# Kernel tuning notes

Measured on AMD Instinct MI355X. Metric: run time of the kernel, lower is better.

Reference implementation:

```python
import jax, jax.numpy as jnp
import numpy as np

N_NODES = 100000
N_EDGES = 1600000
D = 128
BETA = 0.001
EPS = 1e-12  # F.normalize eps


def setup_inputs() -> dict:
    key = jax.random.key(0)
    k1, k2, k3, k4, k5, k6 = jax.random.split(key, 6)
    stdv = 1.0 / np.sqrt(D)
    return {
        "input": jax.random.normal(k1, (N_NODES, D), dtype=jnp.float32),
        "edge_rows": jax.random.randint(k2, (N_EDGES,), 0, N_NODES, dtype=jnp.int32),
        "edge_cols": jax.random.randint(k3, (N_EDGES,), 0, N_NODES, dtype=jnp.int32),
        "edge_vals": jax.random.uniform(k4, (N_EDGES,), dtype=jnp.float32),
        "weight": jax.random.uniform(k5, (D, D), minval=-stdv, maxval=stdv, dtype=jnp.float32),
        "bias": jax.random.uniform(k6, (D,), minval=-stdv, maxval=stdv, dtype=jnp.float32),
    }


def reference(input, edge_rows, edge_cols, edge_vals, weight, bias):
    # dense projection: [N, D]
    support = input @ weight
    # sparse neighbor aggregation: agg[i] = sum_{(i,j) in E} adj_val * support[j]
    msgs = edge_vals[:, None] * support[edge_cols]          # [E, D]
    agg = jax.ops.segment_sum(msgs, edge_rows, num_segments=input.shape[0])
    # beta-weighted residual blend
    out = BETA * input + (1.0 - BETA) * agg
    # row-wise L2 normalize (torch F.normalize, p=2, dim=1)
    norm = jnp.sqrt(jnp.sum(out * out, axis=1, keepdims=True))
    out = out / jnp.maximum(norm, EPS)
    # bias add
    return out + bias
```

## Files before the change

kernel.cpp:

```cpp
#include <hip/hip_runtime.h>

#define N_NODES 100000
#define N_EDGES 1600000
#define D 128
#define NB 1563
#define NSUB 8
#define SUBCAP 224
#define CAP (NSUB*SUBCAP)
#define EPT 8
#define SC_BLOCKS 782
#define CSTRIDE 16

typedef short bf16x8 __attribute__((ext_vector_type(8)));
typedef float f32x4 __attribute__((ext_vector_type(4)));

__device__ __forceinline__ unsigned short f2bf(float x){
  union { float f; unsigned u; } v; v.f = x;
  unsigned r = v.u + 0x7fffu + ((v.u >> 16) & 1u);
  return (unsigned short)(r >> 16);
}

__device__ __forceinline__ float bf2f(unsigned short h){
  union { unsigned u; float f; } v; v.u = ((unsigned)h) << 16;
  return v.f;
}

__global__ __launch_bounds__(256) void convert_input(const float4* __restrict__ in4,
                                                     ushort4* __restrict__ outb,
                                                     const float* __restrict__ W,
                                                     unsigned short* __restrict__ WT){
  int i = blockIdx.x*256 + threadIdx.x;
  if (i < D*D){
    int k = i >> 7, c = i & 127;
    WT[c*128 + k] = f2bf(W[i]);
  }
  float4 a = in4[i];
  ushort4 h;
  h.x = f2bf(a.x); h.y = f2bf(a.y); h.z = f2bf(a.z); h.w = f2bf(a.w);
  outb[i] = h;
}

__global__ __launch_bounds__(256) void scatter_direct(const int4* __restrict__ rows4,
                                                      const int4* __restrict__ cols4,
                                                      const float4* __restrict__ vals4,
                                                      int* __restrict__ cursor,
                                                      int2* __restrict__ edges_s){
  int tid = blockIdx.x*256 + threadIdx.x;
  int base = tid * EPT;
  int s = blockIdx.x & (NSUB-1);
  if (base + EPT <= N_EDGES){
    int4 r0 = rows4[tid*2+0], r1 = rows4[tid*2+1];
    int4 c0 = cols4[tid*2+0], c1 = cols4[tid*2+1];
    float4 v0 = vals4[tid*2+0], v1 = vals4[tid*2+1];
    int r[EPT] = {r0.x, r0.y, r0.z, r0.w, r1.x, r1.y, r1.z, r1.w};
    int c[EPT] = {c0.x, c0.y, c0.z, c0.w, c1.x, c1.y, c1.z, c1.w};
    float v[EPT] = {v0.x, v0.y, v0.z, v0.w, v1.x, v1.y, v1.z, v1.w};
    int pos[EPT];
    #pragma unroll
    for (int k = 0; k < EPT; ++k){
      int b = r[k] >> 6;
      pos[k] = atomicAdd(&cursor[(s*NB + b)*CSTRIDE], 1);
    }
    #pragma unroll
    for (int k = 0; k < EPT; ++k){
      int b = r[k] >> 6;
      if (pos[k] < SUBCAP)
        edges_s[(size_t)b*CAP + s*SUBCAP + pos[k]] =
            make_int2(c[k] | ((r[k] & 63) << 17), __float_as_int(v[k]));
    }
  } else {
    const int* rows = (const int*)rows4;
    const int* cols = (const int*)cols4;
    const float* vals = (const float*)vals4;
    for (int k = 0; k < EPT; ++k){
      int i = base + k;
      if (i >= N_EDGES) break;
      int r = rows[i];
      int b = r >> 6;
      int pos = atomicAdd(&cursor[(s*NB + b)*CSTRIDE], 1);
      if (pos < SUBCAP)
        edges_s[(size_t)b*CAP + s*SUBCAP + pos] =
            make_int2(cols[i] | ((r & 63) << 17), __float_as_int(vals[i]));
    }
  }
}

__global__ __launch_bounds__(512) void agg_final(const ushort4* __restrict__ inb4,
                                                 const int* __restrict__ cursor,
                                                 const int2* __restrict__ edges_g,
                                                 const unsigned short* __restrict__ WTg,
                                                 const float* __restrict__ bias,
                                                 float* __restrict__ out){
  __shared__ unsigned short As[64*136];
  __shared__ int hist[64];
  __shared__ int cur[64];
  __shared__ int rs[64];
  __shared__ int rc[64];
  __shared__ float rsum[2][64];
  int2* st = (int2*)As;

  int t = threadIdx.x;
  int b = blockIdx.x;
  size_t base = (size_t)b * CAP;

  if (t < 64) hist[t] = 0;
  __syncthreads();

  int2 held[NSUB];
  int hv = 0;
  #pragma unroll
  for (int s = 0; s < NSUB; ++s){
    int ms = cursor[(s*NB + b)*CSTRIDE];
    if (ms > SUBCAP) ms = SUBCAP;
    if (t < ms){
      int2 e = edges_g[base + s*SUBCAP + t];
      held[s] = e;
      hv |= (1 << s);
      atomicAdd(&hist[((unsigned)e.x) >> 17], 1);
    }
  }
  __syncthreads();

  if (t < 64){
    int c = hist[t];
    int x = c;
    #pragma unroll
    for (int o = 1; o < 64; o <<= 1){
      int y = __shfl_up(x, o);
      if (t >= o) x += y;
    }
    int excl = x - c;
    cur[t] = excl;
    rs[t] = excl;
    rc[t] = c;
  }
  __syncthreads();

  #pragma unroll
  for (int s = 0; s < NSUB; ++s){
    if (hv & (1 << s)){
      int2 e = held[s];
      int r = ((unsigned)e.x) >> 17;
      int pos = atomicAdd(&cur[r], 1);
      st[pos] = make_int2(e.x & 0x1FFFF, e.y);
    }
  }
  __syncthreads();

  int grp = t >> 5, l = t & 31;
  float4 res[4];
  #pragma unroll
  for (int j = 0; j < 4; ++j){
    int r = grp*4 + j;
    int e = rs[r], end = e + rc[r];
    float4 a0 = make_float4(0.f,0.f,0.f,0.f);
    float4 a1 = make_float4(0.f,0.f,0.f,0.f);
    float4 a2 = make_float4(0.f,0.f,0.f,0.f);
    float4 a3 = make_float4(0.f,0.f,0.f,0.f);
    for (; e + 4 <= end; e += 4){
      int2 e0 = st[e+0];
      int2 e1 = st[e+1];
      int2 e2 = st[e+2];
      int2 e3 = st[e+3];
      ushort4 x0 = inb4[(size_t)e0.x*32 + l];
      ushort4 x1 = inb4[(size_t)e1.x*32 + l];
      ushort4 x2 = inb4[(size_t)e2.x*32 + l];
      ushort4 x3 = inb4[(size_t)e3.x*32 + l];
      float v0 = __int_as_float(e0.y), v1 = __int_as_float(e1.y);
      float v2 = __int_as_float(e2.y), v3 = __int_as_float(e3.y);
      a0.x = fmaf(v0, bf2f(x0.x), a0.x); a0.y = fmaf(v0, bf2f(x0.y), a0.y);
      a0.z = fmaf(v0, bf2f(x0.z), a0.z); a0.w = fmaf(v0, bf2f(x0.w), a0.w);
      a1.x = fmaf(v1, bf2f(x1.x), a1.x); a1.y = fmaf(v1, bf2f(x1.y), a1.y);
      a1.z = fmaf(v1, bf2f(x1.z), a1.z); a1.w = fmaf(v1, bf2f(x1.w), a1.w);
      a2.x = fmaf(v2, bf2f(x2.x), a2.x); a2.y = fmaf(v2, bf2f(x2.y), a2.y);
      a2.z = fmaf(v2, bf2f(x2.z), a2.z); a2.w = fmaf(v2, bf2f(x2.w), a2.w);
      a3.x = fmaf(v3, bf2f(x3.x), a3.x); a3.y = fmaf(v3, bf2f(x3.y), a3.y);
      a3.z = fmaf(v3, bf2f(x3.z), a3.z); a3.w = fmaf(v3, bf2f(x3.w), a3.w);
    }
    for (; e < end; ++e){
      int2 ee = st[e];
      ushort4 x = inb4[(size_t)ee.x*32 + l];
      float v = __int_as_float(ee.y);
      a0.x = fmaf(v, bf2f(x.x), a0.x); a0.y = fmaf(v, bf2f(x.y), a0.y);
      a0.z = fmaf(v, bf2f(x.z), a0.z); a0.w = fmaf(v, bf2f(x.w), a0.w);
    }
    res[j].x = (a0.x + a1.x) + (a2.x + a3.x);
    res[j].y = (a0.y + a1.y) + (a2.y + a3.y);
    res[j].z = (a0.z + a1.z) + (a2.z + a3.z);
    res[j].w = (a0.w + a1.w) + (a2.w + a3.w);
  }
  __syncthreads();

  #pragma unroll
  for (int j = 0; j < 4; ++j){
    int r = grp*4 + j;
    ushort4 h;
    h.x = f2bf(res[j].x); h.y = f2bf(res[j].y);
    h.z = f2bf(res[j].z); h.w = f2bf(res[j].w);
    *((ushort4*)&As[r*136 + l*4]) = h;
  }
  __syncthreads();

  int w = t >> 6, lane = t & 63;
  int wr = w >> 1, wc = w & 1;
  int q = lane >> 4, n = lane & 15;
  bf16x8 afr[4];
  #pragma unroll
  for (int ks = 0; ks < 4; ++ks)
    afr[ks] = *((const bf16x8*)&As[(wr*16 + n)*136 + ks*32 + q*8]);
  __syncthreads();

  int block_row = b * 64;
  #pragma unroll
  for (int i = 0; i < 4; ++i){
    int idx4 = i*512 + t;
    int row = idx4 >> 5, k4 = idx4 & 31;
    int grow = block_row + row;
    ushort4 h = make_ushort4(0,0,0,0);
    if (grow < N_NODES) h = inb4[(size_t)grow*32 + k4];
    *((ushort4*)&As[row*136 + k4*4]) = h;
  }
  __syncthreads();

  f32x4 acc[4];
  #pragma unroll
  for (int ct = 0; ct < 4; ++ct) acc[ct] = (f32x4){0.f, 0.f, 0.f, 0.f};

  #pragma unroll
  for (int ct = 0; ct < 4; ++ct){
    #pragma unroll
    for (int ks = 0; ks < 4; ++ks){
      bf16x8 bfr = *((const bf16x8*)(WTg + (wc*64 + ct*16 + n)*128 + ks*32 + q*8));
      acc[ct] = __builtin_amdgcn_mfma_f32_16x16x32_bf16(afr[ks], bfr, acc[ct], 0, 0, 0);
    }
  }

  float v[4][4];
  float s[4] = {0.f, 0.f, 0.f, 0.f};
  #pragma unroll
  for (int reg = 0; reg < 4; ++reg){
    int row_local = wr*16 + q*4 + reg;
    #pragma unroll
    for (int ct = 0; ct < 4; ++ct){
      float inp = bf2f(As[row_local*136 + wc*64 + ct*16 + n]);
      float val = fmaf(0.999f, acc[ct][reg], 0.001f * inp);
      v[ct][reg] = val;
      s[reg] = fmaf(val, val, s[reg]);
    }
  }
  #pragma unroll
  for (int reg = 0; reg < 4; ++reg){
    float x = s[reg];
    x += __shfl_xor(x, 1);
    x += __shfl_xor(x, 2);
    x += __shfl_xor(x, 4);
    x += __shfl_xor(x, 8);
    s[reg] = x;
  }
  if (n == 0){
    #pragma unroll
    for (int reg = 0; reg < 4; ++reg)
      rsum[wc][wr*16 + q*4 + reg] = s[reg];
  }
  __syncthreads();

  #pragma unroll
  for (int reg = 0; reg < 4; ++reg){
    int row_local = wr*16 + q*4 + reg;
    int grow = block_row + row_local;
    if (grow >= N_NODES) continue;
    float tot = rsum[0][row_local] + rsum[1][row_local];
    float scale = 1.f / fmaxf(sqrtf(tot), 1e-12f);
    float* outrow = out + (size_t)grow * D;
    #pragma unroll
    for (int ct = 0; ct < 4; ++ct){
      int c = wc*64 + ct*16 + n;
      outrow[c] = fmaf(v[ct][reg], scale, bias[c]);
    }
  }
}

extern "C" void kernel_launch(void* const* d_in, const int* in_sizes, int n_in,
                              void* d_out, int out_size, void* d_ws, size_t ws_size,
                              hipStream_t stream){
  const float* input  = (const float*)d_in[0];
  const int*   erows  = (const int*)d_in[1];
  const int*   ecols  = (const int*)d_in[2];
  const float* evals  = (const float*)d_in[3];
  const float* weight = (const float*)d_in[4];
  const float* bias   = (const float*)d_in[5];
  float* out = (float*)d_out;

  int*   cursor    = (int*)d_ws;
  int2*  edges_s   = (int2*)(cursor + NSUB*NB*CSTRIDE);
  ushort4* inb     = (ushort4*)(edges_s + (size_t)NB*CAP);
  unsigned short* WTg = (unsigned short*)(inb + (size_t)N_NODES * 32);

  hipMemsetAsync(cursor, 0, (size_t)NSUB * NB * CSTRIDE * sizeof(int), stream);
  convert_input<<<12500, 256, 0, stream>>>((const float4*)input, inb, weight, WTg);
  scatter_direct<<<SC_BLOCKS, 256, 0, stream>>>((const int4*)erows, (const int4*)ecols,
                                                (const float4*)evals, cursor, edges_s);
  agg_final<<<NB, 512, 0, stream>>>((const ushort4*)inb, cursor, edges_s,
                                    WTg, bias, out);
}
```

Measured before the change: 299.7 us.

## Dynamic row scheduling in aggregation, separate edge smem buffer, unpadded cursors

Each 32-lane group in the aggregation kernel now takes rows from a shared atomic counter instead of a fixed four rows, which balances uneven per-row edge counts across groups. The staged edge list gets its own shared buffer, so results are written straight into the bf16 tile without the extra barrier and register-held results. Cursor counters are no longer padded to separate cache lines, which shrinks the memset but allows atomic contention between neighbouring counters. The larger shared-memory footprint (about 14KB more for the edge array) may lower occupancy.

```diff
diff --git a/kernel.cpp b/kernel.cpp
--- a/kernel.cpp
+++ b/kernel.cpp
@@ -9,7 +9,6 @@
 #define CAP (NSUB*SUBCAP)
 #define EPT 8
 #define SC_BLOCKS 782
-#define CSTRIDE 16
 
 typedef short bf16x8 __attribute__((ext_vector_type(8)));
 typedef float f32x4 __attribute__((ext_vector_type(4)));
@@ -59,7 +58,7 @@
     #pragma unroll
     for (int k = 0; k < EPT; ++k){
       int b = r[k] >> 6;
-      pos[k] = atomicAdd(&cursor[(s*NB + b)*CSTRIDE], 1);
+      pos[k] = atomicAdd(&cursor[s*NB + b], 1);
     }
     #pragma unroll
     for (int k = 0; k < EPT; ++k){
@@ -77,7 +76,7 @@
       if (i >= N_EDGES) break;
       int r = rows[i];
       int b = r >> 6;
-      int pos = atomicAdd(&cursor[(s*NB + b)*CSTRIDE], 1);
+      int pos = atomicAdd(&cursor[s*NB + b], 1);
       if (pos < SUBCAP)
         edges_s[(size_t)b*CAP + s*SUBCAP + pos] =
             make_int2(cols[i] | ((r & 63) << 17), __float_as_int(vals[i]));
@@ -91,26 +90,28 @@
                                                  const unsigned short* __restrict__ WTg,
                                                  const float* __restrict__ bias,
                                                  float* __restrict__ out){
+  __shared__ int2 st[CAP];
   __shared__ unsigned short As[64*136];
   __shared__ int hist[64];
   __shared__ int cur[64];
   __shared__ int rs[64];
   __shared__ int rc[64];
   __shared__ float rsum[2][64];
-  int2* st = (int2*)As;
+  __shared__ int rowctr;
 
   int t = threadIdx.x;
   int b = blockIdx.x;
   size_t base = (size_t)b * CAP;
 
   if (t < 64) hist[t] = 0;
+  if (t == 0) rowctr = 0;
   __syncthreads();
 
   int2 held[NSUB];
   int hv = 0;
   #pragma unroll
   for (int s = 0; s < NSUB; ++s){
-    int ms = cursor[(s*NB + b)*CSTRIDE];
+    int ms = cursor[s*NB + b];
     if (ms > SUBCAP) ms = SUBCAP;
     if (t < ms){
       int2 e = edges_g[base + s*SUBCAP + t];
@@ -147,11 +148,13 @@
   }
   __syncthreads();
 
-  int grp = t >> 5, l = t & 31;
-  float4 res[4];
-  #pragma unroll
-  for (int j = 0; j < 4; ++j){
-    int r = grp*4 + j;
+  int l = t & 31;
+  for (;;){
+    int r = 0;
+    if (l == 0) r = atomicAdd(&rowctr, 1);
+    r = __shfl(r, 0, 32);
+    if (r >= 64) break;
+
     int e = rs[r], end = e + rc[r];
     float4 a0 = make_float4(0.f,0.f,0.f,0.f);
     float4 a1 = make_float4(0.f,0.f,0.f,0.f);
@@ -184,19 +187,14 @@
       a0.x = fmaf(v, bf2f(x.x), a0.x); a0.y = fmaf(v, bf2f(x.y), a0.y);
       a0.z = fmaf(v, bf2f(x.z), a0.z); a0.w = fmaf(v, bf2f(x.w), a0.w);
     }
-    res[j].x = (a0.x + a1.x) + (a2.x + a3.x);
-    res[j].y = (a0.y + a1.y) + (a2.y + a3.y);
-    res[j].z = (a0.z + a1.z) + (a2.z + a3.z);
-    res[j].w = (a0.w + a1.w) + (a2.w + a3.w);
-  }
-  __syncthreads();
-
-  #pragma unroll
-  for (int j = 0; j < 4; ++j){
-    int r = grp*4 + j;
+    float4 sres;
+    sres.x = (a0.x + a1.x) + (a2.x + a3.x);
+    sres.y = (a0.y + a1.y) + (a2.y + a3.y);
+    sres.z = (a0.z + a1.z) + (a2.z + a3.z);
+    sres.w = (a0.w + a1.w) + (a2.w + a3.w);
     ushort4 h;
-    h.x = f2bf(res[j].x); h.y = f2bf(res[j].y);
-    h.z = f2bf(res[j].z); h.w = f2bf(res[j].w);
+    h.x = f2bf(sres.x); h.y = f2bf(sres.y);
+    h.z = f2bf(sres.z); h.w = f2bf(sres.w);
     *((ushort4*)&As[r*136 + l*4]) = h;
   }
   __syncthreads();
@@ -292,11 +290,11 @@
   float* out = (float*)d_out;
 
   int*   cursor    = (int*)d_ws;
-  int2*  edges_s   = (int2*)(cursor + NSUB*NB*CSTRIDE);
+  int2*  edges_s   = (int2*)(cursor + NSUB*NB);
   ushort4* inb     = (ushort4*)(edges_s + (size_t)NB*CAP);
   unsigned short* WTg = (unsigned short*)(inb + (size_t)N_NODES * 32);
 
-  hipMemsetAsync(cursor, 0, (size_t)NSUB * NB * CSTRIDE * sizeof(int), stream);
+  hipMemsetAsync(cursor, 0, (size_t)NSUB * NB * sizeof(int), stream);
   convert_input<<<12500, 256, 0, stream>>>((const float4*)input, inb, weight, WTg);
   scatter_direct<<<SC_BLOCKS, 256, 0, stream>>>((const int4*)erows, (const int4*)ecols,
                                                 (const float4*)evals, cursor, edges_s);
```

New measurement: 321.5 us. 7.3% more time.
